# Kernel tuning notes

Hardware: AMD Instinct MI355X
Metric: run time of the kernel (lower is better)

The kernel has to match this reference:

```python
import jax, jax.numpy as jnp
import numpy as np

EPS = 1e-5       # BatchNorm eps (eval mode, running_mean=0, running_var=1)
TV_F = 1e-5      # FLAGS.tv_reg_factor
CT_F = 1e-4      # FLAGS.constrast_reg_factor


def conv2d(x, w):
    return jax.lax.conv_general_dilated(x, w, (1, 1), 'SAME',
                                        dimension_numbers=('NCHW', 'OIHW', 'NCHW'))


def bn(x, p):
    # eval-mode BN with running_mean=0, running_var=1: x/sqrt(1+eps)*gamma + beta
    g, b = p[0], p[1]
    s = g / jnp.sqrt(1.0 + EPS)
    return x * s[None, :, None, None] + b[None, :, None, None]


def two_conv(x, w1, p1, w2, p2):
    x = jax.nn.relu(bn(conv2d(x, w1), p1))
    return jax.nn.relu(bn(conv2d(x, w2), p2))


def setup_inputs() -> dict:
    key = jax.random.key(0)
    ks = jax.random.split(key, 20)
    B, T, C, H = 8, 16, 2048, 7
    f = lambda k, sh, s=0.02: jax.random.normal(k, sh, jnp.float32) * s
    bnp = lambda k, c: jnp.stack([1.0 + f(k, (c,), 0.05), jnp.zeros((c,), jnp.float32)])
    return {
        'input_x': jax.random.normal(ks[0], (B, C, T, H, H), jnp.float32),
        'mask_w1': f(ks[1], (1024, 2048, 3, 3)), 'mask_bn1': bnp(ks[2], 1024),
        'mask_w2': f(ks[3], (512, 1024, 3, 3)), 'mask_bn2': bnp(ks[4], 512),
        'mask_w3': f(ks[5], (1, 512, 3, 3)),
        'h0_w1': f(ks[6], (1024, 2048, 3, 3)), 'h0_bn1': bnp(ks[7], 1024),
        'h0_w2': f(ks[8], (512, 1024, 3, 3)), 'h0_bn2': bnp(ks[9], 512),
        'c0_w1': f(ks[10], (1024, 2048, 3, 3)), 'c0_bn1': bnp(ks[11], 1024),
        'c0_w2': f(ks[12], (512, 1024, 3, 3)), 'c0_bn2': bnp(ks[13], 512),
        'att_fw': f(ks[14], (1, 2048)), 'att_hw': f(ks[15], (1, 512)),
        'lstm_w': f(ks[16], (4 * 512, 2048 + 512, 3, 3)),
        'lstm_b': jnp.zeros((4 * 512,), jnp.float32),
        'fc_w': f(ks[17], (3, 512)), 'fc_b': jnp.zeros((3,), jnp.float32),
    }


def reference(input_x, mask_w1, mask_bn1, mask_w2, mask_bn2, mask_w3,
              h0_w1, h0_bn1, h0_w2, h0_bn2, c0_w1, c0_bn1, c0_w2, c0_bn2,
              att_fw, att_hw, lstm_w, lstm_b, fc_w, fc_b):
    B, C, T, H, W = input_x.shape
    # dropout_2d is identity in eval mode
    xr = jnp.transpose(input_x, (0, 2, 1, 3, 4)).reshape(B * T, C, H, W)

    # mask conv: 2048 -> 1024 -> 512 -> 1, sigmoid
    m = jax.nn.relu(bn(conv2d(xr, mask_w1), mask_bn1))
    m = jax.nn.relu(bn(conv2d(m, mask_w2), mask_bn2))
    mask = jax.nn.sigmoid(conv2d(m, mask_w3)).reshape(B, T, 1, H, W)

    tv_loss = TV_F * (jnp.sum(jnp.abs(mask[..., 1:] - mask[..., :-1]))
                      + jnp.sum(jnp.abs(mask[..., 1:, :] - mask[..., :-1, :])))
    mA = (mask > 0.5).astype(jnp.float32)
    mB = (mask < 0.5).astype(jnp.float32)
    contrast_loss = (-(mask * mA).mean(0).sum() * CT_F * 0.5
                     + (mask * mB).mean(0).sum() * CT_F * 0.5)

    mx = mask * xr.reshape(B, T, C, H, W)          # (B,T,2048,7,7)
    mean_x = mx.mean(1)                            # (B,2048,7,7)
    h = two_conv(mean_x, h0_w1, h0_bn1, h0_w2, h0_bn2)   # (B,512,7,7)
    c = two_conv(mean_x, c0_w1, c0_bn1, c0_w2, c0_bn2)

    # per-frame feature attention logits (constant across steps)
    att_fea = (mx.mean((3, 4)) @ att_fw.T)[..., 0]       # (B,T)

    def step(carry, _):
        h, c = carry
        att_h = h.mean((2, 3)) @ att_hw.T                # (B,1)
        w = jax.nn.softmax(att_fea + att_h, axis=1)      # (B,T)
        xt = jnp.einsum('btchw,bt->bchw', mx, w)         # attention-weighted frame
        z = conv2d(jnp.concatenate([xt, h], axis=1), lstm_w) + lstm_b[None, :, None, None]
        i, f, o, g = jnp.split(z, 4, axis=1)
        c2 = jax.nn.sigmoid(f) * c + jax.nn.sigmoid(i) * jnp.tanh(g)
        h2 = jax.nn.sigmoid(o) * jnp.tanh(c2)
        return (h2, c2), (h2.mean((2, 3)), w)

    (_, _), (outs, ws) = jax.lax.scan(step, (h, c), None, length=T)
    final_output = outs.mean(0) @ fc_w.T + fc_b          # (B, output_size)
    return final_output, ws[-1], mask, tv_loss, contrast_loss


if __name__ == '__main__':
    out = reference(**setup_inputs())
    print(out[0].shape, out[1].shape, out[2].shape)
```

## Files before the change

kernel.cpp:

```cpp
#include <hip/hip_runtime.h>
#include <cstdint>

typedef unsigned short u16;
typedef __bf16 bf16x8 __attribute__((ext_vector_type(8)));
typedef float f32x4 __attribute__((ext_vector_type(4)));

#define BNRS 0.9999950000374997f

__device__ __forceinline__ u16 f2bf(float f) {
  unsigned u = __float_as_uint(f);
  u += 0x7fffu + ((u >> 16) & 1u);
  return (u16)(u >> 16);
}
__device__ __forceinline__ float bf2f(u16 h) {
  return __uint_as_float(((unsigned)h) << 16);
}

__device__ __forceinline__ void glds16(const u16* g, u16* l) {
  __builtin_amdgcn_global_load_lds(
      (const __attribute__((address_space(1))) void*)g,
      (__attribute__((address_space(3))) void*)l, 16, 0, 0);
}

#define OFF_XN     0ull
#define OFF_M1     42467328ull
#define OFF_M2     63700992ull
#define SZ_M2      10616832ull
#define OFF_MEANX  63700992ull
#define OFF_XTN    66355200ull
#define OFF_TH1    69009408ull
#define OFF_TC1    70336512ull
#define OFF_HN     71663616ull
#define OFF_CST    72327168ull
#define OFF_ZXACC  74317824ull
#define OFF_ATH1   77529088ull
#define OFF_ATC1   79134720ull
#define OFF_ATH2   80740352ull
#define OFF_ATC2   81543168ull
#define OFF_FEA    82345984ull
#define OFF_W      82346496ull
#define OFF_OUTS   82347008ull
#define Z0_END     82378752ull
#define OFF_WA     82378752ull
#define OFF_WB     120127488ull
#define OFF_MX     129564672ull
#define OFF_M1ACC  129564672ull
#define OFF_M2ACC  155254784ull
#define SZ_MACC    38535168ull
#define OFF_LSTMW  82378752ull
#define OFF_ZPART  176750592ull
#define ARENA_END  202440704ull

#define CF_BN    1
#define CF_RELU  2
#define CF_ATOM  4
#define CF_OUTF  8
#define CF_OUTB 16
#define CF_ZOFF 32

__global__ __launch_bounds__(256)
void k_conv(const u16* __restrict__ Xin, const u16* __restrict__ Wt,
            float* __restrict__ outF, u16* __restrict__ outB,
            float* __restrict__ atomF,
            const float* __restrict__ gamma, const float* __restrict__ beta,
            int M, int Cin, int log2Cin, int ldb, int Cout, int kChunk, int flags)
{
  __shared__ u16 As0[4096], As1[4096], Bs0[4096], Bs1[4096];
  const int tid = threadIdx.x;

  int bx = blockIdx.x, by = blockIdx.y, bz = blockIdx.z;
  {
    const int gx = gridDim.x, gy = gridDim.y;
    const int P = gy * gridDim.z;
    if ((P & 7) == 0) {
      int flat = bx + gx * (by + gy * bz);
      int xcd = flat & 7, local = flat >> 3, ppx = P >> 3;
      int x = local / ppx, pl = local - x * ppx;
      int panel = xcd * ppx + pl;
      bx = x; by = panel % gy; bz = panel / gy;
    }
  }
  const int m0 = bx*128, n0 = by*128;
  const int row0 = tid >> 2;
  const int c8 = (((tid & 3) ^ (row0 & 3) ^ ((row0 >> 2) & 3))) * 8;

  long long Abase[2], Bbase[2];
  #pragma unroll
  for (int r = 0; r < 2; ++r) {
    int m = m0 + row0 + r*64; if (m > M-1) m = M-1;
    int img = m / 49, p = m % 49, y = p / 7, xx = p % 7;
    Abase[r] = (long long)(img*81 + y*9 + xx) * Cin + c8;
    Bbase[r] = (long long)(n0 + row0 + r*64) * ldb + c8;
  }
  const long long tapStride = (long long)Cout * ldb;
  const int lane = tid & 63, wave = tid >> 6;
  const int l16 = lane & 15, quad = lane >> 4;
  const int wm = wave & 1, wn = wave >> 1;
  const int fsl = (quad ^ (l16 & 3) ^ ((l16 >> 2) & 3)) * 8;
  const int stg = wave*512;

  f32x4 acc[4][4];
  #pragma unroll
  for (int i=0;i<4;i++)
    #pragma unroll
    for (int j=0;j<4;j++)
      #pragma unroll
      for (int r=0;r<4;r++) acc[i][j][r] = 0.f;

  const int kStart = bz * kChunk, kEnd = kStart + kChunk;

#define STAGE(KK, AB, BB) do {                                            \
    int tap_ = (KK) >> log2Cin;                                           \
    int kc_  = (KK) & (Cin - 1);                                          \
    int ty_  = tap_ / 3;                                                  \
    long long off_ = ((long long)(ty_*6 + tap_) << log2Cin) + kc_;        \
    glds16(Xin + Abase[0] + off_, (AB) + stg);                            \
    glds16(Xin + Abase[1] + off_, (AB) + 2048 + stg);                     \
    const u16* wp_ = Wt + (long long)tap_ * tapStride + kc_;              \
    glds16(wp_ + Bbase[0], (BB) + stg);                                   \
    glds16(wp_ + Bbase[1], (BB) + 2048 + stg);                            \
  } while(0)

#define COMPUTE(AB, BB) do {                                              \
    const u16* Af_ = (AB) + (wm*64 + l16)*32 + fsl;                       \
    const u16* Bf_ = (BB) + (wn*64 + l16)*32 + fsl;                       \
    bf16x8 av[4], bv[4];                                                  \
    _Pragma("unroll")                                                     \
    for (int i=0;i<4;i++) av[i] = *(const bf16x8*)(Af_ + i*512);          \
    _Pragma("unroll")                                                     \
    for (int j=0;j<4;j++) bv[j] = *(const bf16x8*)(Bf_ + j*512);          \
    _Pragma("unroll")                                                     \
    for (int i=0;i<4;i++)                                                 \
      _Pragma("unroll")                                                   \
      for (int j=0;j<4;j++)                                               \
        acc[i][j] = __builtin_amdgcn_mfma_f32_16x16x32_bf16(av[i], bv[j], acc[i][j], 0, 0, 0); \
  } while(0)

  STAGE(kStart, As0, Bs0);
  __syncthreads();
  for (int kk = kStart; kk < kEnd; kk += 64) {
    STAGE(kk + 32, As1, Bs1);
    COMPUTE(As0, Bs0);
    __syncthreads();
    if (kk + 64 < kEnd) STAGE(kk + 64, As0, Bs0);
    COMPUTE(As1, Bs1);
    __syncthreads();
  }
#undef STAGE
#undef COMPUTE

  float* outFz = outF;
  if (flags & CF_ZOFF) outFz = outF + (long long)bz * M * Cout;
  #pragma unroll
  for (int i=0;i<4;i++) {
    #pragma unroll
    for (int r=0;r<4;r++) {
      int m = m0 + wm*64 + i*16 + quad*4 + r;
      if (m >= M) continue;
      int img = m / 49, p = m % 49;
      int pp = (p/7 + 1)*9 + (p%7) + 1;
      #pragma unroll
      for (int j=0;j<4;j++) {
        int n = n0 + wn*64 + j*16 + l16;
        float v = acc[i][j][r];
        if (flags & CF_BN)   v = v * (gamma[n]*BNRS) + beta[n];
        if (flags & CF_RELU) v = fmaxf(v, 0.f);
        if (flags & CF_ATOM) atomicAdd(atomF + (long long)m*Cout + n, v);
        if (flags & CF_OUTF) outFz[(long long)m*Cout + n] = v;
        if (flags & CF_OUTB) outB[((long long)img*81 + pp)*Cout + n] = f2bf(v);
      }
    }
  }
}

__global__ void k_wtrans(const float* __restrict__ W, u16* __restrict__ Wt, int total) {
  int idx = blockIdx.x*256 + threadIdx.x;
  if (idx >= total) return;
  const float* src = W + (long long)idx*9;
  #pragma unroll
  for (int tap=0; tap<9; ++tap)
    Wt[(long long)tap*total + idx] = f2bf(src[tap]);
}

__global__ void k_transpose(const float* __restrict__ x, u16* __restrict__ Xn) {
  int idx = blockIdx.x*256 + threadIdx.x;
  int p = idx % 49; int r = idx / 49; int c8 = (r & 255)*8; int b = r >> 8;
  if (b >= 8) return;
  int pp = (p/7 + 1)*9 + (p%7) + 1;
  for (int t=0; t<16; ++t) {
    u16 o[8];
    #pragma unroll
    for (int j=0;j<8;j++)
      o[j] = f2bf(x[((long long)(b*2048 + c8 + j)*16 + t)*49 + p]);
    *(uint4*)&Xn[((long long)(b*16+t)*81 + pp)*2048 + c8] = *(uint4*)o;
  }
}

__global__ void k_mask3(const u16* __restrict__ M2b, const float* __restrict__ w3,
                        float* __restrict__ maskOut) {
  int img = blockIdx.x / 49, p = blockIdx.x % 49;
  int y = p/7, xx = p%7;
  int lane = threadIdx.x;
  float s = 0.f;
  for (int k = lane; k < 4608; k += 64) {
    int tap = k >> 9, c = k & 511;
    int ty = tap/3, tx = tap - ty*3;
    int pp = (y+ty)*9 + xx + tx;
    s += bf2f(M2b[((long long)img*81 + pp)*512 + c]) * w3[c*9 + tap];
  }
  #pragma unroll
  for (int off=32; off>0; off>>=1) s += __shfl_down(s, off, 64);
  if (lane == 0) maskOut[blockIdx.x] = 1.f/(1.f + expf(-s));
}

__global__ void k_losses(const float* __restrict__ mk, float* __restrict__ dout) {
  __shared__ float s1[256], s2[256];
  int tid = threadIdx.x;
  float tv = 0.f, ct = 0.f;
  for (int i = tid; i < 128*7*6; i += 256) {
    int img = i / 42, r = i % 42, y = r / 6, xx = r % 6;
    int base = img*49 + y*7 + xx;
    tv += fabsf(mk[base+1] - mk[base]);
  }
  for (int i = tid; i < 128*6*7; i += 256) {
    int img = i / 42, r = i % 42, y = r / 7, xx = r % 7;
    int base = img*49 + y*7 + xx;
    tv += fabsf(mk[base+7] - mk[base]);
  }
  for (int i = tid; i < 6272; i += 256) {
    float v = mk[i];
    ct += (v < 0.5f ? v : 0.f) - (v > 0.5f ? v : 0.f);
  }
  s1[tid] = tv; s2[tid] = ct; __syncthreads();
  for (int off=128; off>0; off>>=1) {
    if (tid < off) { s1[tid]+=s1[tid+off]; s2[tid]+=s2[tid+off]; }
    __syncthreads();
  }
  if (tid==0) { dout[6424] = 1e-5f * s1[0]; dout[6425] = (1e-4f*0.5f/8.f) * s2[0]; }
}

__global__ void k_mx(const float* __restrict__ x, const float* __restrict__ mk,
                     u16* __restrict__ mxn, u16* __restrict__ meanx) {
  int idx = blockIdx.x*256 + threadIdx.x;
  int p = idx % 49; int r = idx / 49; int c8 = (r & 255)*8; int b = r >> 8;
  if (b >= 8) return;
  int pp = (p/7+1)*9 + (p%7) + 1;
  float macc[8] = {0,0,0,0,0,0,0,0};
  for (int t=0;t<16;++t) {
    float mval = mk[(b*16+t)*49 + p];
    u16 o[8];
    #pragma unroll
    for (int j=0;j<8;j++) {
      float v = x[((long long)(b*2048 + c8 + j)*16 + t)*49 + p] * mval;
      o[j] = f2bf(v); macc[j] += v;
    }
    *(uint4*)&mxn[((long long)(b*16+t)*81 + pp)*2048 + c8] = *(uint4*)o;
  }
  u16 o2[8];
  #pragma unroll
  for (int j=0;j<8;j++) o2[j] = f2bf(macc[j] * (1.f/16.f));
  *(uint4*)&meanx[((long long)b*81 + pp)*2048 + c8] = *(uint4*)o2;
}

__global__ void k_att(const u16* __restrict__ mxn, const float* __restrict__ fw,
                      float* __restrict__ fea) {
  __shared__ float red[256];
  int img = blockIdx.x, tid = threadIdx.x;
  const u16* base = mxn + (long long)img*81*2048;
  float s = 0.f;
  for (int k = tid; k < 49*2048; k += 256) {
    int p = k >> 11, c = k & 2047;
    int pp = (p/7+1)*9 + (p%7) + 1;
    s += bf2f(base[(long long)pp*2048 + c]) * fw[c];
  }
  red[tid] = s; __syncthreads();
  for (int off=128; off>0; off>>=1) { if (tid<off) red[tid]+=red[tid+off]; __syncthreads(); }
  if (tid==0) fea[img] = red[0] * (1.f/49.f);
}

__global__ void k_softmax(const float* __restrict__ fea, float* __restrict__ w,
                          float* __restrict__ doutW) {
  int b = threadIdx.x;
  if (b >= 8) return;
  float mx = -1e30f;
  for (int t=0;t<16;t++) mx = fmaxf(mx, fea[b*16+t]);
  float e[16], s = 0.f;
  for (int t=0;t<16;t++) { e[t] = expf(fea[b*16+t]-mx); s += e[t]; }
  float inv = 1.f/s;
  for (int t=0;t<16;t++) { float v = e[t]*inv; w[b*16+t] = v; doutW[b*16+t] = v; }
}

__global__ void k_xt(const u16* __restrict__ mxn, const float* __restrict__ w,
                     u16* __restrict__ xtn) {
  int idx = blockIdx.x*256 + threadIdx.x;
  int c8 = (idx & 255)*8; int r = idx >> 8; int p = r % 49; int b = r / 49;
  if (b >= 8) return;
  int pp = (p/7+1)*9 + (p%7)+1;
  float a[8] = {0,0,0,0,0,0,0,0};
  for (int t=0;t<16;t++) {
    float wt = w[b*16+t];
    uint4 raw = *(const uint4*)&mxn[((long long)(b*16+t)*81 + pp)*2048 + c8];
    const u16* h = (const u16*)&raw;
    #pragma unroll
    for (int j=0;j<8;j++) a[j] += wt * bf2f(h[j]);
  }
  u16 o[8];
  #pragma unroll
  for (int j=0;j<8;j++) o[j] = f2bf(a[j]);
  *(uint4*)&xtn[((long long)b*81+pp)*2048 + c8] = *(uint4*)o;
}

__global__ void k_finalize(const float* __restrict__ acc, const float* __restrict__ bn,
                           u16* __restrict__ outB, float* __restrict__ outF,
                           int C, int nImg) {
  int idx = blockIdx.x*256 + threadIdx.x;
  int total = nImg*81*C;
  if (idx >= total) return;
  int c = idx % C; int r = idx / C; int pp = r % 81; int img = r / 81;
  int py = pp/9, px = pp%9;
  bool inter = (py>=1 && py<=7 && px>=1 && px<=7);
  float v = 0.f;
  int m = img*49 + (py-1)*7 + (px-1);
  if (inter) {
    v = acc[(long long)m*C + c];
    v = v*(bn[c]*BNRS) + bn[C+c];
    v = fmaxf(v, 0.f);
  }
  if (outB) outB[idx] = f2bf(v);
  if (outF && inter) outF[(long long)m*C + c] = v;
}

__global__ void k_gate(const float* __restrict__ zx, const float* __restrict__ zp,
                       const float* __restrict__ lb, float* __restrict__ cst,
                       u16* __restrict__ hn, float* __restrict__ outs) {
  int idx = blockIdx.x*256 + threadIdx.x;
  if (idx >= 392*512) return;
  int c = idx & 511; int m = idx >> 9;
  int b = m / 49, p = m % 49;
  int pp = (p/7+1)*9 + (p%7)+1;
  const float* zr = zx + (long long)m*2048;
  float zi = zr[c]        + lb[c];
  float zf = zr[c+512]    + lb[c+512];
  float zo = zr[c+1024]   + lb[c+1024];
  float zg = zr[c+1536]   + lb[c+1536];
  #pragma unroll
  for (int s=0;s<8;s++) {
    const float* q = zp + ((long long)s*392 + m)*2048;
    zi += q[c]; zf += q[c+512]; zo += q[c+1024]; zg += q[c+1536];
  }
  float si = 1.f/(1.f+expf(-zi));
  float sf = 1.f/(1.f+expf(-zf));
  float so = 1.f/(1.f+expf(-zo));
  float cn = sf*cst[idx] + si*tanhf(zg);
  float h  = so*tanhf(cn);
  cst[idx] = cn;
  hn[((long long)b*81 + pp)*512 + c] = f2bf(h);
  atomicAdd(outs + b*512 + c, h*(1.f/784.f));
}

__global__ void k_fc(const float* __restrict__ outs, const float* __restrict__ fcw,
                     const float* __restrict__ fcb, float* __restrict__ dout) {
  int t = threadIdx.x;
  if (t >= 24) return;
  int b = t / 3, j = t % 3;
  float s = fcb[j];
  for (int c=0;c<512;c++) s += outs[b*512+c]*fcw[j*512+c];
  dout[b*3+j] = s;
}

extern "C" void kernel_launch(void* const* d_in, const int* in_sizes, int n_in,
                              void* d_out, int out_size, void* d_ws, size_t ws_size,
                              hipStream_t stream) {
  (void)in_sizes; (void)n_in; (void)out_size;
  const float* x        = (const float*)d_in[0];
  const float* mask_w1  = (const float*)d_in[1];
  const float* mask_bn1 = (const float*)d_in[2];
  const float* mask_w2  = (const float*)d_in[3];
  const float* mask_bn2 = (const float*)d_in[4];
  const float* mask_w3  = (const float*)d_in[5];
  const float* h0_w1    = (const float*)d_in[6];
  const float* h0_bn1   = (const float*)d_in[7];
  const float* h0_w2    = (const float*)d_in[8];
  const float* h0_bn2   = (const float*)d_in[9];
  const float* c0_w1    = (const float*)d_in[10];
  const float* c0_bn1   = (const float*)d_in[11];
  const float* c0_w2    = (const float*)d_in[12];
  const float* c0_bn2   = (const float*)d_in[13];
  const float* att_fw   = (const float*)d_in[14];
  const float* lstm_w   = (const float*)d_in[16];
  const float* lstm_b   = (const float*)d_in[17];
  const float* fc_w     = (const float*)d_in[18];
  const float* fc_b     = (const float*)d_in[19];
  float* dout = (float*)d_out;
  char* ws = (char*)d_ws;
  if (ws_size < ARENA_END) return;

  u16* XN    = (u16*)(ws + OFF_XN);
  u16* M1b   = (u16*)(ws + OFF_M1);
  u16* M2b   = (u16*)(ws + OFF_M2);
  u16* MEANX = (u16*)(ws + OFF_MEANX);
  u16* XTN   = (u16*)(ws + OFF_XTN);
  u16* TH1   = (u16*)(ws + OFF_TH1);
  u16* TC1   = (u16*)(ws + OFF_TC1);
  u16* HN    = (u16*)(ws + OFF_HN);
  float* CST   = (float*)(ws + OFF_CST);
  float* ZXACC = (float*)(ws + OFF_ZXACC);
  float* ATH1  = (float*)(ws + OFF_ATH1);
  float* ATC1  = (float*)(ws + OFF_ATC1);
  float* ATH2  = (float*)(ws + OFF_ATH2);
  float* ATC2  = (float*)(ws + OFF_ATC2);
  float* FEA   = (float*)(ws + OFF_FEA);
  float* Wbuf  = (float*)(ws + OFF_W);
  float* OUTS  = (float*)(ws + OFF_OUTS);
  u16* WA    = (u16*)(ws + OFF_WA);
  u16* WB    = (u16*)(ws + OFF_WB);
  u16* MX    = (u16*)(ws + OFF_MX);
  u16* LSTMW = (u16*)(ws + OFF_LSTMW);
  float* ZPART = (float*)(ws + OFF_ZPART);
  float* M1ACC = (float*)(ws + OFF_M1ACC);
  float* M2ACC = (float*)(ws + OFF_M2ACC);

  hipMemsetAsync(ws, 0, (size_t)Z0_END, stream);
  hipMemsetAsync(ws + OFF_M1ACC, 0, (size_t)SZ_MACC, stream);

  k_wtrans<<<8192, 256, 0, stream>>>(mask_w1, WA, 1024*2048);
  k_wtrans<<<2048, 256, 0, stream>>>(mask_w2, WB, 512*1024);
  k_transpose<<<392, 256, 0, stream>>>(x, XN);
  k_conv<<<dim3(49,8,4),256,0,stream>>>(XN, WA, nullptr, nullptr, M1ACC,
      nullptr, nullptr, 6272, 2048, 11, 2048, 1024, 4608, CF_ATOM);
  k_finalize<<<41472, 256, 0, stream>>>(M1ACC, mask_bn1, M1b, nullptr, 1024, 128);
  k_conv<<<dim3(49,4,4),256,0,stream>>>(M1b, WB, nullptr, nullptr, M2ACC,
      nullptr, nullptr, 6272, 1024, 10, 1024, 512, 2304, CF_ATOM);
  k_finalize<<<20736, 256, 0, stream>>>(M2ACC, mask_bn2, M2b, nullptr, 512, 128);
  k_mask3<<<6272, 64, 0, stream>>>(M2b, mask_w3, dout+152);
  k_losses<<<1, 256, 0, stream>>>(dout+152, dout);

  hipMemsetAsync(ws + OFF_M2, 0, (size_t)SZ_M2, stream);
  k_mx<<<392, 256, 0, stream>>>(x, dout+152, MX, MEANX);
  k_att<<<128, 256, 0, stream>>>(MX, att_fw, FEA);
  k_softmax<<<1, 64, 0, stream>>>(FEA, Wbuf, dout+24);
  k_xt<<<392, 256, 0, stream>>>(MX, Wbuf, XTN);

  k_wtrans<<<8192, 256, 0, stream>>>(h0_w1, WA, 1024*2048);
  k_wtrans<<<2048, 256, 0, stream>>>(h0_w2, WB, 512*1024);
  k_conv<<<dim3(4,8,16),256,0,stream>>>(MEANX, WA, nullptr, nullptr, ATH1,
      nullptr, nullptr, 392, 2048, 11, 2048, 1024, 1152, CF_ATOM);
  k_finalize<<<2592, 256, 0, stream>>>(ATH1, h0_bn1, TH1, nullptr, 1024, 8);
  k_conv<<<dim3(4,4,16),256,0,stream>>>(TH1, WB, nullptr, nullptr, ATH2,
      nullptr, nullptr, 392, 1024, 10, 1024, 512, 576, CF_ATOM);
  k_finalize<<<1296, 256, 0, stream>>>(ATH2, h0_bn2, HN, nullptr, 512, 8);

  k_wtrans<<<8192, 256, 0, stream>>>(c0_w1, WA, 1024*2048);
  k_wtrans<<<2048, 256, 0, stream>>>(c0_w2, WB, 512*1024);
  k_conv<<<dim3(4,8,16),256,0,stream>>>(MEANX, WA, nullptr, nullptr, ATC1,
      nullptr, nullptr, 392, 2048, 11, 2048, 1024, 1152, CF_ATOM);
  k_finalize<<<2592, 256, 0, stream>>>(ATC1, c0_bn1, TC1, nullptr, 1024, 8);
  k_conv<<<dim3(4,4,16),256,0,stream>>>(TC1, WB, nullptr, nullptr, ATC2,
      nullptr, nullptr, 392, 1024, 10, 1024, 512, 576, CF_ATOM);
  k_finalize<<<1296, 256, 0, stream>>>(ATC2, c0_bn2, nullptr, CST, 512, 8);

  k_wtrans<<<20480, 256, 0, stream>>>(lstm_w, LSTMW, 2048*2560);
  k_conv<<<dim3(4,16,16),256,0,stream>>>(XTN, LSTMW, nullptr, nullptr, ZXACC,
      nullptr, nullptr, 392, 2048, 11, 2560, 2048, 1152, CF_ATOM);
  for (int step = 0; step < 16; ++step) {
    k_conv<<<dim3(4,16,8),256,0,stream>>>(HN, LSTMW+2048, ZPART, nullptr, nullptr,
        nullptr, nullptr, 392, 512, 9, 2560, 2048, 576, CF_OUTF|CF_ZOFF);
    k_gate<<<784, 256, 0, stream>>>(ZXACC, ZPART, lstm_b, CST, HN, OUTS);
  }
  k_fc<<<1, 64, 0, stream>>>(OUTS, fc_w, fc_b, dout);
}
```

Before: 2.072 ms.

## Triple-buffer conv GEMM LDS staging with explicit vmcnt waits

Replaces the double-buffered LDS pipeline in the implicit-GEMM conv kernel with a three-stage ring, so loads run two K-steps ahead. Full __syncthreads are swapped for explicit s_waitcnt vmcnt plus s_barrier, letting newer global-to-LDS loads stay in flight while compute proceeds. The aim is to hide global load latency and reduce stalls at barriers. The cost is more LDS per block, which may reduce occupancy. The loop also assumes the per-chunk iteration count is a multiple of three.

```diff
diff --git a/kernel.cpp b/kernel.cpp
--- a/kernel.cpp
+++ b/kernel.cpp
@@ -65,7 +65,8 @@
             const float* __restrict__ gamma, const float* __restrict__ beta,
             int M, int Cin, int log2Cin, int ldb, int Cout, int kChunk, int flags)
 {
-  __shared__ u16 As0[4096], As1[4096], Bs0[4096], Bs1[4096];
+  __shared__ u16 As[3*4096];
+  __shared__ u16 Bs[3*4096];
   const int tid = threadIdx.x;
 
   int bx = blockIdx.x, by = blockIdx.y, bz = blockIdx.z;
@@ -107,11 +108,17 @@
       #pragma unroll
       for (int r=0;r<4;r++) acc[i][j][r] = 0.f;
 
-  const int kStart = bz * kChunk, kEnd = kStart + kChunk;
-
-#define STAGE(KK, AB, BB) do {                                            \
-    int tap_ = (KK) >> log2Cin;                                           \
-    int kc_  = (KK) & (Cin - 1);                                          \
+  const int kStart = bz * kChunk;
+  const int nIter = kChunk >> 5;
+
+#define VW4 asm volatile("s_waitcnt vmcnt(4)" ::: "memory")
+#define VW0 asm volatile("s_waitcnt vmcnt(0)" ::: "memory")
+#define BARX __builtin_amdgcn_s_barrier()
+
+#define STAGE(IT, AB, BB) do {                                            \
+    int kk_ = kStart + (IT)*32;                                           \
+    int tap_ = kk_ >> log2Cin;                                            \
+    int kc_  = kk_ & (Cin - 1);                                           \
     int ty_  = tap_ / 3;                                                  \
     long long off_ = ((long long)(ty_*6 + tap_) << log2Cin) + kc_;        \
     glds16(Xin + Abase[0] + off_, (AB) + stg);                            \
@@ -136,18 +143,25 @@
         acc[i][j] = __builtin_amdgcn_mfma_f32_16x16x32_bf16(av[i], bv[j], acc[i][j], 0, 0, 0); \
   } while(0)
 
-  STAGE(kStart, As0, Bs0);
-  __syncthreads();
-  for (int kk = kStart; kk < kEnd; kk += 64) {
-    STAGE(kk + 32, As1, Bs1);
-    COMPUTE(As0, Bs0);
-    __syncthreads();
-    if (kk + 64 < kEnd) STAGE(kk + 64, As0, Bs0);
-    COMPUTE(As1, Bs1);
-    __syncthreads();
+  STAGE(0, As + 0,    Bs + 0);
+  STAGE(1, As + 4096, Bs + 4096);
+  for (int it = 0; it < nIter; it += 3) {
+    VW4; BARX;
+    if (it + 2 < nIter) STAGE(it + 2, As + 8192, Bs + 8192);
+    COMPUTE(As + 0, Bs + 0);
+    VW4; BARX;
+    if (it + 3 < nIter) STAGE(it + 3, As + 0, Bs + 0);
+    COMPUTE(As + 4096, Bs + 4096);
+    if (it + 3 < nIter) { VW4; } else { VW0; }
+    BARX;
+    if (it + 4 < nIter) STAGE(it + 4, As + 4096, Bs + 4096);
+    COMPUTE(As + 8192, Bs + 8192);
   }
 #undef STAGE
 #undef COMPUTE
+#undef VW4
+#undef VW0
+#undef BARX
 
   float* outFz = outF;
   if (flags & CF_ZOFF) outFz = outF + (long long)bz * M * Cout;
```

Measured after the change: 2.213 ms. 6.8% more time.
